# Kernel optimization log

Hardware: AMD Instinct MI355X
Metric: run time of the kernel (lower is better)

## Reference

```python
import jax, jax.numpy as jnp
import numpy as np

N_NODES = 100000
N_FEAT = 512
HIDDEN = 16
OUT = 2
N_EDGES = 3200000


def gcn_conv(x, edge_index, W, b, n_nodes):
    """PyG-style GCNConv: h = D^-1/2 (A+I) D^-1/2 (x W) + b."""
    h = x @ W  # project first (PyG order) -> [N, out]
    src, dst = edge_index[0], edge_index[1]
    # add self loops
    loop = jnp.arange(n_nodes, dtype=src.dtype)
    src = jnp.concatenate([src, loop])
    dst = jnp.concatenate([dst, loop])
    # symmetric normalization: deg = in-degree (scatter ones to dst)
    deg = jax.ops.segment_sum(jnp.ones_like(dst, dtype=h.dtype), dst, num_segments=n_nodes)
    dinv = jax.lax.rsqrt(deg)  # deg >= 1 due to self loops
    norm = dinv[src] * dinv[dst]  # [E+N]
    msg = h[src] * norm[:, None]  # gather + scale
    out = jax.ops.segment_sum(msg, dst, num_segments=n_nodes)  # scatter-add
    return out + b


def setup_inputs() -> dict:
    key = jax.random.key(0)
    k1, k2, k3, k4, k5 = jax.random.split(key, 5)
    x = jax.random.normal(k1, (N_NODES, N_FEAT), dtype=jnp.float32)
    edge_index = jax.random.randint(k2, (2, N_EDGES), 0, N_NODES, dtype=jnp.int64)
    # Glorot-style params for the two GCNConv layers
    W1 = jax.random.normal(k3, (N_FEAT, HIDDEN), dtype=jnp.float32) / np.sqrt(N_FEAT)
    b1 = jnp.zeros((HIDDEN,), dtype=jnp.float32)
    W2 = jax.random.normal(k4, (HIDDEN, OUT), dtype=jnp.float32) / np.sqrt(HIDDEN)
    b2 = jnp.zeros((OUT,), dtype=jnp.float32)
    return {"x": x, "edge_index": edge_index, "W1": W1, "b1": b1, "W2": W2, "b2": b2}


def reference(x, edge_index, W1, b1, W2, b2):
    n = x.shape[0]
    h = gcn_conv(x, edge_index, W1, b1, n)
    h = jax.nn.relu(h)
    out = gcn_conv(h, edge_index, W2, b2, n)
    return out
```

## Files before the change

### kernel.cpp

```cpp
#include <hip/hip_runtime.h>
#include <hip/hip_fp16.h>

#define NFEAT 512
#define HID 16
#define MAXNB 512
#define NBLK 512
#define PACK_SHIFT 17
#define PACK_MASK ((1 << PACK_SHIFT) - 1)

typedef _Float16 f16x8 __attribute__((ext_vector_type(8)));
typedef float f32x4 __attribute__((ext_vector_type(4)));

__device__ __forceinline__ void gemm_tile(const float* __restrict__ x,
                                          const float* __restrict__ W,
                                          __half* __restrict__ h1u,
                                          int tile, int N, int lane) {
  const int n = lane & 15;
  const int g = lane >> 4;

  f16x8 bf[16];
#pragma unroll
  for (int f = 0; f < 16; ++f) {
    const float* wp = W + (size_t)(f * 32 + g * 8) * HID + n;
#pragma unroll
    for (int j = 0; j < 8; ++j) bf[f][j] = (_Float16)wp[j * HID];
  }

  int rowbase = tile * 16;
  if (rowbase + 16 > N) rowbase = N - 16;
  const float* xr = x + (size_t)(rowbase + n) * NFEAT + g * 8;

  f32x4 acc = {0.f, 0.f, 0.f, 0.f};
#pragma unroll
  for (int f = 0; f < 16; ++f) {
    float4 p0 = *(const float4*)(xr + f * 32);
    float4 p1 = *(const float4*)(xr + f * 32 + 4);
    f16x8 af;
    af[0] = (_Float16)p0.x; af[1] = (_Float16)p0.y;
    af[2] = (_Float16)p0.z; af[3] = (_Float16)p0.w;
    af[4] = (_Float16)p1.x; af[5] = (_Float16)p1.y;
    af[6] = (_Float16)p1.z; af[7] = (_Float16)p1.w;
    acc = __builtin_amdgcn_mfma_f32_16x16x32_f16(af, bf[f], acc, 0, 0, 0);
  }

#pragma unroll
  for (int r = 0; r < 4; ++r) {
    int row = rowbase + g * 4 + r;
    h1u[(size_t)row * HID + n] = __float2half(acc[r]);
  }
}

__global__ __launch_bounds__(512) void k_hist_gemm(const int* __restrict__ ei,
                                                   int* __restrict__ cnt_t,
                                                   int E, int nb,
                                                   const float* __restrict__ x,
                                                   const float* __restrict__ W,
                                                   __half* __restrict__ h1u,
                                                   int N, int tsplit) {
  __shared__ int l[MAXNB];
  if (blockIdx.x < NBLK) {
    for (int i = threadIdx.x; i < nb; i += 512) l[i] = 0;
    __syncthreads();
    int chunk = (E + NBLK - 1) / NBLK;
    int beg = blockIdx.x * chunk;
    int end = beg + chunk; if (end > E) end = E;
    for (int e = beg + threadIdx.x; e < end; e += 512)
      atomicAdd(&l[ei[(size_t)E + e] >> 8], 1);
    __syncthreads();
    for (int b = threadIdx.x; b < nb; b += 512)
      cnt_t[(size_t)b * NBLK + blockIdx.x] = l[b];
  } else {
    int tile = (blockIdx.x - NBLK) * 8 + (threadIdx.x >> 6);
    if (tile < tsplit) gemm_tile(x, W, h1u, tile, N, threadIdx.x & 63);
  }
}

__global__ __launch_bounds__(64) void k_colscan(const int* __restrict__ cnt_t,
                                                int* __restrict__ off_t,
                                                int* __restrict__ gcnt, int nb) {
  int b = blockIdx.x;
  if (b >= nb) return;
  int lane = threadIdx.x;
  int4 v0 = *(const int4*)&cnt_t[(size_t)b * NBLK + lane * 8];
  int4 v1 = *(const int4*)&cnt_t[(size_t)b * NBLK + lane * 8 + 4];
  int tot = (v0.x + v0.y + v0.z + v0.w) + (v1.x + v1.y + v1.z + v1.w);
  int s = tot;
  for (int d = 1; d < 64; d <<= 1) {
    int o = __shfl_up(s, d);
    if (lane >= d) s += o;
  }
  int excl = s - tot;
  int4 w0, w1;
  w0.x = excl;
  w0.y = w0.x + v0.x;
  w0.z = w0.y + v0.y;
  w0.w = w0.z + v0.z;
  w1.x = w0.w + v0.w;
  w1.y = w1.x + v1.x;
  w1.z = w1.y + v1.y;
  w1.w = w1.z + v1.z;
  *(int4*)&off_t[(size_t)b * NBLK + lane * 8] = w0;
  *(int4*)&off_t[(size_t)b * NBLK + lane * 8 + 4] = w1;
  if (lane == 63) gcnt[b] = s;
}

__global__ __launch_bounds__(512) void k_bscan(const int* __restrict__ gcnt,
                                               int* __restrict__ gbase, int nb) {
  __shared__ int sm[512];
  int t = threadIdx.x;
  int c = (t < nb) ? gcnt[t] : 0;
  int pc = (c + 15) & ~15;
  sm[t] = pc;
  __syncthreads();
  for (int off = 1; off < 512; off <<= 1) {
    int x = (t >= off) ? sm[t - off] : 0;
    __syncthreads();
    sm[t] += x;
    __syncthreads();
  }
  if (t < nb) gbase[t] = sm[t] - pc;
}

__global__ __launch_bounds__(512) void k_scatter_gemm(const int* __restrict__ ei,
                                                      const int* __restrict__ gbase,
                                                      const int* __restrict__ off_t,
                                                      int* __restrict__ binned,
                                                      int E, int nb,
                                                      const float* __restrict__ x,
                                                      const float* __restrict__ W,
                                                      __half* __restrict__ h1u,
                                                      int N, int tsplit, int ntiles) {
  __shared__ int cur[MAXNB];
  if (blockIdx.x < NBLK) {
    for (int b = threadIdx.x; b < nb; b += 512)
      cur[b] = gbase[b] + off_t[(size_t)b * NBLK + blockIdx.x];
    __syncthreads();
    int chunk = (E + NBLK - 1) / NBLK;
    int beg = blockIdx.x * chunk;
    int end = beg + chunk; if (end > E) end = E;
    for (int e = beg + threadIdx.x; e < end; e += 512) {
      int s = ei[e];
      int d = ei[(size_t)E + e];
      int b = d >> 8;
      int pos = atomicAdd(&cur[b], 1);
      binned[pos] = s | ((d & 255) << PACK_SHIFT);
    }
  } else {
    int tile = tsplit + (blockIdx.x - NBLK) * 8 + (threadIdx.x >> 6);
    if (tile < ntiles) gemm_tile(x, W, h1u, tile, N, threadIdx.x & 63);
  }
}

__global__ __launch_bounds__(512) void k_sortbucket(const int* __restrict__ gbase,
                                                    const int* __restrict__ gcnt,
                                                    const int* __restrict__ binned,
                                                    int* __restrict__ csr,
                                                    int* __restrict__ rowbeg,
                                                    int* __restrict__ rowend,
                                                    float* __restrict__ dinv,
                                                    __half* __restrict__ h1h, int N) {
  __shared__ int hist[256];
  __shared__ int sm[256];
  __shared__ int cur[256];
  __shared__ float sdinv[256];
  const int t = threadIdx.x;
  const int b = blockIdx.x;
  const int base = gbase[b], cnt = gcnt[b];
  if (t < 256) hist[t] = 0;
  __syncthreads();
  for (int j = base + t; j < base + cnt; j += 512)
    atomicAdd(&hist[binned[j] >> PACK_SHIFT], 1);
  __syncthreads();
  int h = 0;
  if (t < 256) {
    h = hist[t];
    sm[t] = h;
  }
  __syncthreads();
  for (int off = 1; off < 256; off <<= 1) {
    int x = 0;
    if (t < 256 && t >= off) x = sm[t - off];
    __syncthreads();
    if (t < 256) sm[t] += x;
    __syncthreads();
  }
  if (t < 256) {
    int incl = sm[t];
    int excl = incl - h;
    cur[t] = excl;
    float dv = rsqrtf((float)h + 1.0f);
    sdinv[t] = dv;
    int node = b * 256 + t;
    if (node < N) {
      rowbeg[node] = base + excl;
      rowend[node] = base + incl;
      dinv[node] = dv;
    }
  }
  __syncthreads();
  for (int j = base + t; j < base + cnt; j += 512) {
    int val = binned[j];
    int pos = atomicAdd(&cur[val >> PACK_SHIFT], 1);
    csr[base + pos] = val & PACK_MASK;
  }
  {
    int node = b * 256 + (t >> 1);
    if (node < N) {
      float dv = sdinv[t >> 1];
      __half* hp = h1h + (size_t)node * HID + (t & 1) * 8;
      f16x8 v = *(const f16x8*)hp;
#pragma unroll
      for (int j = 0; j < 8; ++j) v[j] = (_Float16)((float)v[j] * dv);
      *(f16x8*)hp = v;
    }
  }
}

__global__ __launch_bounds__(256) void k_agg1f(const int* __restrict__ rowbeg,
                                               const int* __restrict__ rowend,
                                               const int* __restrict__ csr,
                                               const __half* __restrict__ h1h,
                                               const float* __restrict__ dinv,
                                               const float* __restrict__ b1,
                                               const float* __restrict__ W2,
                                               float* __restrict__ h2s, int N) {
  const int f = threadIdx.x & 15;
  const int node = blockIdx.x * 16 + (threadIdx.x >> 4);
  if (node >= N) return;
  int j = rowbeg[node];
  const int end = rowend[node];
  float acc = __half2float(h1h[(size_t)node * HID + f]);
  for (; j < end && (j & 3); ++j) acc += __half2float(h1h[(size_t)csr[j] * HID + f]);
  for (; j + 8 <= end; j += 8) {
    int4 s0 = *(const int4*)&csr[j];
    int4 s1 = *(const int4*)&csr[j + 4];
    float a0 = __half2float(h1h[(size_t)s0.x * HID + f]);
    float a1 = __half2float(h1h[(size_t)s0.y * HID + f]);
    float a2 = __half2float(h1h[(size_t)s0.z * HID + f]);
    float a3 = __half2float(h1h[(size_t)s0.w * HID + f]);
    float a4 = __half2float(h1h[(size_t)s1.x * HID + f]);
    float a5 = __half2float(h1h[(size_t)s1.y * HID + f]);
    float a6 = __half2float(h1h[(size_t)s1.z * HID + f]);
    float a7 = __half2float(h1h[(size_t)s1.w * HID + f]);
    acc += ((a0 + a1) + (a2 + a3)) + ((a4 + a5) + (a6 + a7));
  }
  for (; j + 4 <= end; j += 4) {
    int4 ss = *(const int4*)&csr[j];
    float a0 = __half2float(h1h[(size_t)ss.x * HID + f]);
    float a1 = __half2float(h1h[(size_t)ss.y * HID + f]);
    float a2 = __half2float(h1h[(size_t)ss.z * HID + f]);
    float a3 = __half2float(h1h[(size_t)ss.w * HID + f]);
    acc += (a0 + a1) + (a2 + a3);
  }
  for (; j < end; ++j) acc += __half2float(h1h[(size_t)csr[j] * HID + f]);

  float di = dinv[node];
  float v = fmaxf(acc * di + b1[f], 0.f);
  float o0 = v * W2[f * 2 + 0];
  float o1 = v * W2[f * 2 + 1];
#pragma unroll
  for (int d = 1; d < 16; d <<= 1) {
    o0 += __shfl_xor(o0, d);
    o1 += __shfl_xor(o1, d);
  }
  if (f == 0) *(float2*)&h2s[(size_t)node * 2] = make_float2(o0 * di, o1 * di);
}

__global__ __launch_bounds__(256) void k_agg2f(const int* __restrict__ rowbeg,
                                               const int* __restrict__ rowend,
                                               const int* __restrict__ csr,
                                               const float* __restrict__ h2s,
                                               const float* __restrict__ dinv,
                                               const float* __restrict__ b2,
                                               float* __restrict__ out, int N) {
  int i = blockIdx.x * 256 + threadIdx.x;
  if (i >= N) return;
  int j = rowbeg[i];
  const int end = rowend[i];
  float2 o = *(const float2*)&h2s[(size_t)i * 2];
  for (; j < end && (j & 3); ++j) {
    float2 v = *(const float2*)&h2s[(size_t)csr[j] * 2];
    o.x += v.x; o.y += v.y;
  }
  for (; j + 8 <= end; j += 8) {
    int4 s0 = *(const int4*)&csr[j];
    int4 s1 = *(const int4*)&csr[j + 4];
    float2 v0 = *(const float2*)&h2s[(size_t)s0.x * 2];
    float2 v1 = *(const float2*)&h2s[(size_t)s0.y * 2];
    float2 v2 = *(const float2*)&h2s[(size_t)s0.z * 2];
    float2 v3 = *(const float2*)&h2s[(size_t)s0.w * 2];
    float2 v4 = *(const float2*)&h2s[(size_t)s1.x * 2];
    float2 v5 = *(const float2*)&h2s[(size_t)s1.y * 2];
    float2 v6 = *(const float2*)&h2s[(size_t)s1.z * 2];
    float2 v7 = *(const float2*)&h2s[(size_t)s1.w * 2];
    o.x += ((v0.x + v1.x) + (v2.x + v3.x)) + ((v4.x + v5.x) + (v6.x + v7.x));
    o.y += ((v0.y + v1.y) + (v2.y + v3.y)) + ((v4.y + v5.y) + (v6.y + v7.y));
  }
  for (; j + 4 <= end; j += 4) {
    int4 ss = *(const int4*)&csr[j];
    float2 v0 = *(const float2*)&h2s[(size_t)ss.x * 2];
    float2 v1 = *(const float2*)&h2s[(size_t)ss.y * 2];
    float2 v2 = *(const float2*)&h2s[(size_t)ss.z * 2];
    float2 v3 = *(const float2*)&h2s[(size_t)ss.w * 2];
    o.x += (v0.x + v1.x) + (v2.x + v3.x);
    o.y += (v0.y + v1.y) + (v2.y + v3.y);
  }
  for (; j < end; ++j) {
    float2 v = *(const float2*)&h2s[(size_t)csr[j] * 2];
    o.x += v.x; o.y += v.y;
  }
  float di = dinv[i];
  o.x = o.x * di + b2[0];
  o.y = o.y * di + b2[1];
  *(float2*)&out[(size_t)i * 2] = o;
}

extern "C" void kernel_launch(void* const* d_in, const int* in_sizes, int n_in,
                              void* d_out, int out_size, void* d_ws, size_t ws_size,
                              hipStream_t stream) {
  const float* x = (const float*)d_in[0];
  const int* ei = (const int*)d_in[1];
  const float* W1 = (const float*)d_in[2];
  const float* b1 = (const float*)d_in[3];
  const float* W2 = (const float*)d_in[4];
  const float* b2 = (const float*)d_in[5];
  float* out = (float*)d_out;
  const int N = in_sizes[0] / NFEAT;
  const int E = in_sizes[1] / 2;
  const int nb = (N + 255) / 256;

  char* p = (char*)d_ws;
  int* cnt_t = (int*)p;    p += (size_t)MAXNB * NBLK * 4;
  int* off_t = (int*)p;    p += (size_t)MAXNB * NBLK * 4;
  int* gcnt = (int*)p;     p += (size_t)MAXNB * 4;
  int* gbase = (int*)p;    p += (size_t)MAXNB * 4;
  int* binned = (int*)p;   p += ((size_t)E + MAXNB * 16) * 4;
  int* csr = (int*)p;      p += ((size_t)E + MAXNB * 16) * 4;
  int* rowbeg = (int*)p;   p += (size_t)N * 4;
  int* rowend = (int*)p;   p += (size_t)N * 4;
  float* dinv = (float*)p; p += (size_t)N * 4;
  __half* h1h = (__half*)p; p += (size_t)N * HID * 2;
  float* h2s = (float*)p;  p += (size_t)N * 2 * 4;

  const int ntiles = (N + 15) / 16;
  const int tsplit = ((ntiles / 2) + 7) & ~7;
  const int gA = (tsplit + 7) / 8;
  const int gB = (ntiles - tsplit + 7) / 8;

  k_hist_gemm<<<NBLK + gA, 512, 0, stream>>>(ei, cnt_t, E, nb, x, W1, h1h, N, tsplit);
  k_colscan<<<nb, 64, 0, stream>>>(cnt_t, off_t, gcnt, nb);
  k_bscan<<<1, 512, 0, stream>>>(gcnt, gbase, nb);
  k_scatter_gemm<<<NBLK + gB, 512, 0, stream>>>(ei, gbase, off_t, binned, E, nb,
                                                x, W1, h1h, N, tsplit, ntiles);
  k_sortbucket<<<nb, 512, 0, stream>>>(gbase, gcnt, binned, csr, rowbeg, rowend,
                                       dinv, h1h, N);
  k_agg1f<<<(N + 15) / 16, 256, 0, stream>>>(rowbeg, rowend, csr, h1h, dinv, b1, W2, h2s, N);
  k_agg2f<<<(N + 255) / 256, 256, 0, stream>>>(rowbeg, rowend, csr, h2s, dinv, b2, out, N);
}
```

Measured before the change: 166.3 us.

## Fold bucket base scan into consumers, pack column scans, split agg2 across lanes

Removes the single-block k_bscan launch by recomputing the bucket-base prefix sum in LDS inside both k_scatter_gemm and k_sortbucket. Packs eight column scans per 512-thread block instead of one 64-thread block each. Rewrites the layer-2 aggregation to use four lanes per node with shuffle reduction, giving more memory-level parallelism for the gathers. The redundant per-block scan adds work and barriers to every block, and the final sum order changes slightly.

```diff
diff --git a/kernel.cpp b/kernel.cpp
--- a/kernel.cpp
+++ b/kernel.cpp
@@ -75,12 +75,12 @@
   }
 }
 
-__global__ __launch_bounds__(64) void k_colscan(const int* __restrict__ cnt_t,
-                                                int* __restrict__ off_t,
-                                                int* __restrict__ gcnt, int nb) {
-  int b = blockIdx.x;
+__global__ __launch_bounds__(512) void k_scan(const int* __restrict__ cnt_t,
+                                              int* __restrict__ off_t,
+                                              int* __restrict__ gcnt, int nb) {
+  int b = blockIdx.x * 8 + (threadIdx.x >> 6);
   if (b >= nb) return;
-  int lane = threadIdx.x;
+  int lane = threadIdx.x & 63;
   int4 v0 = *(const int4*)&cnt_t[(size_t)b * NBLK + lane * 8];
   int4 v1 = *(const int4*)&cnt_t[(size_t)b * NBLK + lane * 8 + 4];
   int tot = (v0.x + v0.y + v0.z + v0.w) + (v1.x + v1.y + v1.z + v1.w);
@@ -104,13 +104,12 @@
   if (lane == 63) gcnt[b] = s;
 }
 
-__global__ __launch_bounds__(512) void k_bscan(const int* __restrict__ gcnt,
-                                               int* __restrict__ gbase, int nb) {
-  __shared__ int sm[512];
+__device__ __forceinline__ void bscan_lds(const int* __restrict__ gcnt, int nb,
+                                          int* sm , int& my_pc) {
   int t = threadIdx.x;
   int c = (t < nb) ? gcnt[t] : 0;
-  int pc = (c + 15) & ~15;
-  sm[t] = pc;
+  my_pc = (c + 15) & ~15;
+  sm[t] = my_pc;
   __syncthreads();
   for (int off = 1; off < 512; off <<= 1) {
     int x = (t >= off) ? sm[t - off] : 0;
@@ -118,11 +117,10 @@
     sm[t] += x;
     __syncthreads();
   }
-  if (t < nb) gbase[t] = sm[t] - pc;
 }
 
 __global__ __launch_bounds__(512) void k_scatter_gemm(const int* __restrict__ ei,
-                                                      const int* __restrict__ gbase,
+                                                      const int* __restrict__ gcnt,
                                                       const int* __restrict__ off_t,
                                                       int* __restrict__ binned,
                                                       int E, int nb,
@@ -131,9 +129,12 @@
                                                       __half* __restrict__ h1u,
                                                       int N, int tsplit, int ntiles) {
   __shared__ int cur[MAXNB];
+  __shared__ int sm[512];
   if (blockIdx.x < NBLK) {
-    for (int b = threadIdx.x; b < nb; b += 512)
-      cur[b] = gbase[b] + off_t[(size_t)b * NBLK + blockIdx.x];
+    int my_pc;
+    bscan_lds(gcnt, nb, sm, my_pc);
+    int t = threadIdx.x;
+    if (t < nb) cur[t] = (sm[t] - my_pc) + off_t[(size_t)t * NBLK + blockIdx.x];
     __syncthreads();
     int chunk = (E + NBLK - 1) / NBLK;
     int beg = blockIdx.x * chunk;
@@ -151,21 +152,30 @@
   }
 }
 
-__global__ __launch_bounds__(512) void k_sortbucket(const int* __restrict__ gbase,
-                                                    const int* __restrict__ gcnt,
+__global__ __launch_bounds__(512) void k_sortbucket(const int* __restrict__ gcnt,
                                                     const int* __restrict__ binned,
                                                     int* __restrict__ csr,
                                                     int* __restrict__ rowbeg,
                                                     int* __restrict__ rowend,
                                                     float* __restrict__ dinv,
-                                                    __half* __restrict__ h1h, int N) {
+                                                    __half* __restrict__ h1h,
+                                                    int nb, int N) {
+  __shared__ int smg[512];
   __shared__ int hist[256];
   __shared__ int sm[256];
   __shared__ int cur[256];
   __shared__ float sdinv[256];
+  __shared__ int sbase;
   const int t = threadIdx.x;
   const int b = blockIdx.x;
-  const int base = gbase[b], cnt = gcnt[b];
+  {
+    int my_pc;
+    bscan_lds(gcnt, nb, smg, my_pc);
+    if (t == b) sbase = smg[t] - my_pc;
+    __syncthreads();
+  }
+  const int base = sbase;
+  const int cnt = gcnt[b];
   if (t < 256) hist[t] = 0;
   __syncthreads();
   for (int j = base + t; j < base + cnt; j += 512)
@@ -273,46 +283,28 @@
                                                const float* __restrict__ dinv,
                                                const float* __restrict__ b2,
                                                float* __restrict__ out, int N) {
-  int i = blockIdx.x * 256 + threadIdx.x;
-  if (i >= N) return;
-  int j = rowbeg[i];
-  const int end = rowend[i];
-  float2 o = *(const float2*)&h2s[(size_t)i * 2];
-  for (; j < end && (j & 3); ++j) {
-    float2 v = *(const float2*)&h2s[(size_t)csr[j] * 2];
-    o.x += v.x; o.y += v.y;
-  }
-  for (; j + 8 <= end; j += 8) {
-    int4 s0 = *(const int4*)&csr[j];
-    int4 s1 = *(const int4*)&csr[j + 4];
-    float2 v0 = *(const float2*)&h2s[(size_t)s0.x * 2];
-    float2 v1 = *(const float2*)&h2s[(size_t)s0.y * 2];
-    float2 v2 = *(const float2*)&h2s[(size_t)s0.z * 2];
-    float2 v3 = *(const float2*)&h2s[(size_t)s0.w * 2];
-    float2 v4 = *(const float2*)&h2s[(size_t)s1.x * 2];
-    float2 v5 = *(const float2*)&h2s[(size_t)s1.y * 2];
-    float2 v6 = *(const float2*)&h2s[(size_t)s1.z * 2];
-    float2 v7 = *(const float2*)&h2s[(size_t)s1.w * 2];
-    o.x += ((v0.x + v1.x) + (v2.x + v3.x)) + ((v4.x + v5.x) + (v6.x + v7.x));
-    o.y += ((v0.y + v1.y) + (v2.y + v3.y)) + ((v4.y + v5.y) + (v6.y + v7.y));
-  }
-  for (; j + 4 <= end; j += 4) {
-    int4 ss = *(const int4*)&csr[j];
-    float2 v0 = *(const float2*)&h2s[(size_t)ss.x * 2];
-    float2 v1 = *(const float2*)&h2s[(size_t)ss.y * 2];
-    float2 v2 = *(const float2*)&h2s[(size_t)ss.z * 2];
-    float2 v3 = *(const float2*)&h2s[(size_t)ss.w * 2];
-    o.x += (v0.x + v1.x) + (v2.x + v3.x);
-    o.y += (v0.y + v1.y) + (v2.y + v3.y);
-  }
-  for (; j < end; ++j) {
-    float2 v = *(const float2*)&h2s[(size_t)csr[j] * 2];
-    o.x += v.x; o.y += v.y;
-  }
-  float di = dinv[i];
-  o.x = o.x * di + b2[0];
-  o.y = o.y * di + b2[1];
-  *(float2*)&out[(size_t)i * 2] = o;
+  const int l = threadIdx.x & 3;
+  const int node = blockIdx.x * 64 + (threadIdx.x >> 2);
+  if (node >= N) return;
+  const int beg = rowbeg[node];
+  const int end = rowend[node];
+  float ox = 0.f, oy = 0.f;
+  for (int j = beg + l; j < end; j += 4) {
+    int s = csr[j];
+    float2 v = *(const float2*)&h2s[(size_t)s * 2];
+    ox += v.x;
+    oy += v.y;
+  }
+  ox += __shfl_xor(ox, 1); oy += __shfl_xor(oy, 1);
+  ox += __shfl_xor(ox, 2); oy += __shfl_xor(oy, 2);
+  if (l == 0) {
+    float2 self = *(const float2*)&h2s[(size_t)node * 2];
+    float di = dinv[node];
+    float2 o;
+    o.x = (ox + self.x) * di + b2[0];
+    o.y = (oy + self.y) * di + b2[1];
+    *(float2*)&out[(size_t)node * 2] = o;
+  }
 }
 
 extern "C" void kernel_launch(void* const* d_in, const int* in_sizes, int n_in,
@@ -333,7 +325,6 @@
   int* cnt_t = (int*)p;    p += (size_t)MAXNB * NBLK * 4;
   int* off_t = (int*)p;    p += (size_t)MAXNB * NBLK * 4;
   int* gcnt = (int*)p;     p += (size_t)MAXNB * 4;
-  int* gbase = (int*)p;    p += (size_t)MAXNB * 4;
   int* binned = (int*)p;   p += ((size_t)E + MAXNB * 16) * 4;
   int* csr = (int*)p;      p += ((size_t)E + MAXNB * 16) * 4;
   int* rowbeg = (int*)p;   p += (size_t)N * 4;
@@ -348,12 +339,11 @@
   const int gB = (ntiles - tsplit + 7) / 8;
 
   k_hist_gemm<<<NBLK + gA, 512, 0, stream>>>(ei, cnt_t, E, nb, x, W1, h1h, N, tsplit);
-  k_colscan<<<nb, 64, 0, stream>>>(cnt_t, off_t, gcnt, nb);
-  k_bscan<<<1, 512, 0, stream>>>(gcnt, gbase, nb);
-  k_scatter_gemm<<<NBLK + gB, 512, 0, stream>>>(ei, gbase, off_t, binned, E, nb,
+  k_scan<<<(nb + 7) / 8, 512, 0, stream>>>(cnt_t, off_t, gcnt, nb);
+  k_scatter_gemm<<<NBLK + gB, 512, 0, stream>>>(ei, gcnt, off_t, binned, E, nb,
                                                 x, W1, h1h, N, tsplit, ntiles);
-  k_sortbucket<<<nb, 512, 0, stream>>>(gbase, gcnt, binned, csr, rowbeg, rowend,
-                                       dinv, h1h, N);
+  k_sortbucket<<<nb, 512, 0, stream>>>(gcnt, binned, csr, rowbeg, rowend,
+                                       dinv, h1h, nb, N);
   k_agg1f<<<(N + 15) / 16, 256, 0, stream>>>(rowbeg, rowend, csr, h1h, dinv, b1, W2, h2s, N);
-  k_agg2f<<<(N + 255) / 256, 256, 0, stream>>>(rowbeg, rowend, csr, h2s, dinv, b2, out, N);
-}
+  k_agg2f<<<(N + 63) / 64, 256, 0, stream>>>(rowbeg, rowend, csr, h2s, dinv, b2, out, N);
+}
```

New measurement: 170.3 us. 1.02x slower.
